# Kernel optimization log

Hardware: AMD Instinct MI355X
Metric: run time of the kernel (lower is better)

The kernel has to match this reference:

```python
import jax, jax.numpy as jnp
import numpy as np
from jax.experimental.ode import odeint

TOL = 1.0  # ODEBlock default: rtol = atol = tol


def _odefunc(x, t, W1, b1, W2, b2):
    # time-concat MLP: f(x, t) = tanh([x, t] @ W1 + b1) @ W2 + b2
    tcol = jnp.full((x.shape[0], 1), t, dtype=x.dtype)  # [B, 1]
    h = jnp.tanh(jnp.concatenate([x, tcol], axis=1) @ W1 + b1)  # [B, H]
    return h @ W2 + b2  # [B, D]


def setup_inputs() -> dict:
    key = jax.random.key(0)
    k1, k2, k3 = jax.random.split(key, 3)
    B, D, H = 4096, 2048, 2048
    # scale weights so the dynamics stay well-conditioned over t in [0,1]
    x = jax.random.normal(k1, (B, D), dtype=jnp.float32)
    W1 = jax.random.normal(k2, (D + 1, H), dtype=jnp.float32) / np.sqrt(D + 1)
    b1 = jnp.zeros((H,), dtype=jnp.float32)
    W2 = jax.random.normal(k3, (H, D), dtype=jnp.float32) / np.sqrt(H)
    b2 = jnp.zeros((D,), dtype=jnp.float32)
    return {"x": x, "W1": W1, "b1": b1, "W2": W2, "b2": b2}


def reference(x, W1, b1, W2, b2):
    f = lambda y, t: _odefunc(y, t, W1, b1, W2, b2)
    ts = jnp.array([0.0, 1.0], dtype=jnp.float32)
    states = odeint(f, x, ts, rtol=TOL, atol=TOL)  # [2, B, D]
    return states[-1]
```

## Files before the change

kernel.cpp:

```cpp
#include <hip/hip_runtime.h>

typedef unsigned short u16;
typedef __attribute__((ext_vector_type(8))) short short8;
typedef __attribute__((ext_vector_type(4))) float floatx4;
typedef __attribute__((ext_vector_type(4))) unsigned short ushortx4;

#define BD 4096
#define DD 2048
#define NTOT (BD*DD)
#define MAX_STEPS 3

#define CE0 ((float)(35.0/384.0 - 1951.0/21600.0))
#define CE2 ((float)(500.0/1113.0 - 22642.0/50085.0))
#define CE3 ((float)(125.0/192.0 - 451.0/720.0))
#define CE4 ((float)(-2187.0/6784.0 + 12231.0/42400.0))
#define CE5 ((float)(11.0/84.0 - 649.0/6300.0))
#define CE6 ((float)(-1.0/60.0))

#define CM0 ((float)(6025192743.0/30085553152.0/2.0))
#define CM2 ((float)(51252292925.0/65400821598.0/2.0))
#define CM3 ((float)(-2691868925.0/45128329728.0/2.0))
#define CM4 ((float)(187940372067.0/1594534317056.0/2.0))
#define CM5 ((float)(-1776094331.0/19743644256.0/2.0))
#define CM6 ((float)(11237099.0/235043384.0/2.0))

#define CS0 ((float)(35.0/384.0))
#define CS2 ((float)(500.0/1113.0))
#define CS3 ((float)(125.0/192.0))
#define CS4 ((float)(-2187.0/6784.0))
#define CS5 ((float)(11.0/84.0))

#define B50 ((float)(9017.0/3168.0))
#define B51 ((float)(-355.0/33.0))
#define B52 ((float)(46732.0/5247.0))
#define B53 ((float)(49.0/176.0))
#define B54 ((float)(-5103.0/18656.0))

struct Scal {
  float t, dt, last_t, h0, dt_saved;
  float d0s, d1s, d2s, errs;
  float d0, d1;
  int run_flag, accept_flag, cur;
};

__device__ __forceinline__ u16 f2bf(float x) {
  unsigned int u = __float_as_uint(x);
  u += 0x7FFFu + ((u >> 16) & 1u);
  return (u16)(u >> 16);
}
__device__ __forceinline__ float bf2f(u16 h) {
  return __uint_as_float(((unsigned int)h) << 16);
}
__device__ __forceinline__ void splitw(float v, u16* oh, u16* ol, size_t idx) {
  u16 h = f2bf(v);
  oh[idx] = h;
  ol[idx] = f2bf(v - bf2f(h));
}
__device__ __forceinline__ void splitw4(floatx4 v, u16* oh, u16* ol, size_t idx) {
  ushortx4 h, l;
  #pragma unroll
  for (int e = 0; e < 4; ++e) {
    u16 hh = f2bf(v[e]);
    h[e] = hh;
    l[e] = f2bf(v[e] - bf2f(hh));
  }
  *(ushortx4*)&oh[idx] = h;
  *(ushortx4*)&ol[idx] = l;
}

__device__ __forceinline__ void gload16(const u16* g, u16* l) {
  __builtin_amdgcn_global_load_lds(
      (const __attribute__((address_space(1))) void*)g,
      (__attribute__((address_space(3))) void*)l, 16, 0, 0);
}

__global__ void transpose_hi(const float* __restrict__ W, u16* __restrict__ th,
                             int K, int N) {
  __shared__ float tile[32][33];
  int k0 = blockIdx.x * 32, n0 = blockIdx.y * 32;
  int tx = threadIdx.x, ty = threadIdx.y;
  #pragma unroll
  for (int j = 0; j < 32; j += 8)
    tile[ty + j][tx] = W[(size_t)(k0 + ty + j) * N + n0 + tx];
  __syncthreads();
  #pragma unroll
  for (int j = 0; j < 32; j += 8) {
    int nn = ty + j, kk = tx;
    th[(size_t)(n0 + nn) * K + k0 + kk] = f2bf(tile[kk][nn]);
  }
}

template <int STAGE>
__global__ __launch_bounds__(256, 2)
void gemm_fused(const u16* __restrict__ Ah, const u16* __restrict__ Al,
                const u16* __restrict__ Bt,
                const float* __restrict__ bias, const float* __restrict__ trow,
                int tmode, float alpha_c,
                float bb0, float bb1, float bb2, float bbv,
                float* __restrict__ YA, float* __restrict__ YB,
                float* __restrict__ F,
                float* __restrict__ K2M, float* __restrict__ K3,
                float* __restrict__ K4,
                u16* __restrict__ oh, u16* __restrict__ ol,
                Scal* __restrict__ s, int flag) {
  if (flag == 1 && !s->run_flag) return;

  __shared__ __attribute__((aligned(16))) u16 raw[2][16384];
  #define AH_OFF 0
  #define AL_OFF 4096
  #define B_OFF  8192

  const int tid = threadIdx.x;
  const int lane = tid & 63;
  const int wave = tid >> 6;

  const int lin = blockIdx.x;
  const int xcd = lin & 7;
  const int slot = lin >> 3;
  const int bm = (xcd * 8 + (slot >> 4)) * 64;
  const int bn = (slot & 15) * 128;

  const int m_w = (wave >> 1) * 32;
  const int n_w = (wave & 1) * 64;
  const int lr = lane & 15;

  const int lrow = lane >> 3;
  const int lcol = (((lane & 7) ^ (lane >> 3)) << 3);
  const int ra = wave * 16;
  const int rb = wave * 32;
  const u16* gAh = Ah + (size_t)(bm + ra + lrow) * DD + lcol;
  const u16* gAl = Al + (size_t)(bm + ra + lrow) * DD + lcol;
  const u16* gB  = Bt + (size_t)(bn + rb + lrow) * DD + lcol;

  floatx4 acc[2][4];
  #pragma unroll
  for (int i = 0; i < 2; ++i)
    #pragma unroll
    for (int j = 0; j < 4; ++j)
      acc[i][j] = (floatx4){0.f, 0.f, 0.f, 0.f};

  auto stage = [&](int k0, int b) {
    #pragma unroll
    for (int t = 0; t < 2; ++t) {
      gload16(gAh + k0 + (size_t)(8 * t) * DD, &raw[b][AH_OFF + (ra + 8 * t) * 64]);
      gload16(gAl + k0 + (size_t)(8 * t) * DD, &raw[b][AL_OFF + (ra + 8 * t) * 64]);
    }
    #pragma unroll
    for (int t = 0; t < 4; ++t)
      gload16(gB + k0 + (size_t)(8 * t) * DD, &raw[b][B_OFF + (rb + 8 * t) * 64]);
  };

  stage(0, 0);
  stage(64, 1);
  asm volatile("s_waitcnt vmcnt(8)" ::: "memory");
  __builtin_amdgcn_s_barrier();

  const int NT = DD / 64;
  int bufc = 0;
  for (int t = 0; t < NT; ++t) {
    #pragma unroll
    for (int kk = 0; kk < 2; ++kk) {
      const int cb = kk * 4 + (lane >> 4);
      short8 afh[2], afl[2], bfv[4];
      #pragma unroll
      for (int i = 0; i < 2; ++i) {
        int r = m_w + i * 16 + lr;
        int ar = r * 64 + ((cb ^ (lr & 7)) << 3);
        afh[i] = *(const short8*)&raw[bufc][AH_OFF + ar];
        afl[i] = *(const short8*)&raw[bufc][AL_OFF + ar];
      }
      #pragma unroll
      for (int j = 0; j < 4; ++j) {
        int r = n_w + j * 16 + lr;
        bfv[j] = *(const short8*)&raw[bufc][B_OFF + r * 64 + ((cb ^ (lr & 7)) << 3)];
      }
      #pragma unroll
      for (int i = 0; i < 2; ++i)
        #pragma unroll
        for (int j = 0; j < 4; ++j) {
          acc[i][j] = __builtin_amdgcn_mfma_f32_16x16x32_bf16(afh[i], bfv[j], acc[i][j], 0, 0, 0);
          acc[i][j] = __builtin_amdgcn_mfma_f32_16x16x32_bf16(afl[i], bfv[j], acc[i][j], 0, 0, 0);
        }
    }

    if (t < NT - 1) {
      __builtin_amdgcn_s_barrier();
      if (t < NT - 2) {
        stage((t + 2) * 64, bufc);
        asm volatile("s_waitcnt vmcnt(8)" ::: "memory");
      } else {
        asm volatile("s_waitcnt vmcnt(0)" ::: "memory");
      }
      __builtin_amdgcn_s_barrier();
      bufc ^= 1;
    }
  }

  const int cur = s->cur;
  const float* Yc = cur ? YB : YA;
  float* NY = cur ? YA : YB;
  const float dt = s->dt;
  float tj = 0.f;
  if (STAGE == 100) tj = (tmode == 0) ? (s->t + dt * alpha_c) : s->h0;

  __syncthreads();
  float* ep = (float*)&raw[0][0];
  const int oq = (lane >> 4) * 4;
  const int oc = lane & 15;
  #pragma unroll
  for (int i = 0; i < 2; ++i)
    #pragma unroll
    for (int j = 0; j < 4; ++j)
      #pragma unroll
      for (int r = 0; r < 4; ++r)
        ep[(m_w + i * 16 + oq + r) * 132 + (n_w + j * 16 + oc)] = acc[i][j][r];
  __syncthreads();

  float err_acc = 0.f;
  #pragma unroll
  for (int q = 0; q < 8; ++q) {
    const int fidx = tid + 256 * q;
    const int rl = fidx >> 5;
    const int cl = (fidx & 31) << 2;
    const int n = bn + cl;
    const size_t idx = (size_t)(bm + rl) * DD + n;
    floatx4 v = *(const floatx4*)&ep[rl * 132 + cl];
    {
      floatx4 b4 = *(const floatx4*)&bias[n];
      #pragma unroll
      for (int e = 0; e < 4; ++e) v[e] = v[e] + b4[e];
    }
    if constexpr (STAGE == 100) {
      floatx4 t4 = *(const floatx4*)&trow[n];
      floatx4 h4;
      #pragma unroll
      for (int e = 0; e < 4; ++e) h4[e] = tanhf(v[e] + tj * t4[e]);
      splitw4(h4, oh, ol, idx);
    } else if constexpr (STAGE == 0) {
      floatx4 fv = *(const floatx4*)&F[idx];
      floatx4 yv = *(const floatx4*)&Yc[idx];
      *(floatx4*)&K2M[idx] = v;
      floatx4 ys;
      #pragma unroll
      for (int e = 0; e < 4; ++e)
        ys[e] = yv[e] + dt * (bb0 * fv[e] + bbv * v[e]);
      splitw4(ys, oh, ol, idx);
    } else if constexpr (STAGE == 1) {
      floatx4 fv = *(const floatx4*)&F[idx];
      floatx4 yv = *(const floatx4*)&Yc[idx];
      floatx4 k2 = *(const floatx4*)&K2M[idx];
      *(floatx4*)&K3[idx] = v;
      floatx4 ys;
      #pragma unroll
      for (int e = 0; e < 4; ++e)
        ys[e] = yv[e] + dt * (bb0 * fv[e] + bb1 * k2[e] + bbv * v[e]);
      splitw4(ys, oh, ol, idx);
    } else if constexpr (STAGE == 2) {
      floatx4 fv = *(const floatx4*)&F[idx];
      floatx4 yv = *(const floatx4*)&Yc[idx];
      floatx4 k2 = *(const floatx4*)&K2M[idx];
      floatx4 k3 = *(const floatx4*)&K3[idx];
      *(floatx4*)&K4[idx] = v;
      floatx4 ys;
      #pragma unroll
      for (int e = 0; e < 4; ++e)
        ys[e] = yv[e] + dt * (bb0 * fv[e] + bb1 * k2[e] + bb2 * k3[e] + bbv * v[e]);
      splitw4(ys, oh, ol, idx);
    } else if constexpr (STAGE == 3) {
      floatx4 fv = *(const floatx4*)&F[idx];
      floatx4 yv = *(const floatx4*)&Yc[idx];
      floatx4 k2 = *(const floatx4*)&K2M[idx];
      floatx4 k3 = *(const floatx4*)&K3[idx];
      floatx4 k4 = *(const floatx4*)&K4[idx];
      *(floatx4*)&K2M[idx] = v;
      floatx4 ys;
      #pragma unroll
      for (int e = 0; e < 4; ++e)
        ys[e] = yv[e] + dt * (B50 * fv[e] + B51 * k2[e] + B52 * k3[e] + B53 * k4[e] + B54 * v[e]);
      splitw4(ys, oh, ol, idx);
    } else if constexpr (STAGE == 4) {
      floatx4 fv = *(const floatx4*)&F[idx];
      floatx4 yv = *(const floatx4*)&Yc[idx];
      floatx4 k3 = *(const floatx4*)&K3[idx];
      floatx4 k4 = *(const floatx4*)&K4[idx];
      floatx4 k5 = *(const floatx4*)&K2M[idx];
      floatx4 ny, E4, M4;
      #pragma unroll
      for (int e = 0; e < 4; ++e) {
        ny[e] = yv[e] + dt * (CS0 * fv[e] + CS2 * k3[e] + CS3 * k4[e] + CS4 * k5[e] + CS5 * v[e]);
        E4[e] = CE0 * fv[e] + CE2 * k3[e] + CE3 * k4[e] + CE4 * k5[e] + CE5 * v[e];
        M4[e] = CM0 * fv[e] + CM2 * k3[e] + CM3 * k4[e] + CM4 * k5[e] + CM5 * v[e];
      }
      *(floatx4*)&NY[idx] = ny;
      *(floatx4*)&K3[idx] = E4;
      *(floatx4*)&K2M[idx] = M4;
      splitw4(ny, oh, ol, idx);
    } else if constexpr (STAGE == 5) {
      floatx4 E4 = *(const floatx4*)&K3[idx];
      floatx4 M4 = *(const floatx4*)&K2M[idx];
      floatx4 yv = *(const floatx4*)&Yc[idx];
      floatx4 nyv = *(const floatx4*)&NY[idx];
      floatx4 Ef, Mf;
      #pragma unroll
      for (int e = 0; e < 4; ++e) {
        Ef[e] = E4[e] + CE6 * v[e];
        Mf[e] = M4[e] + CM6 * v[e];
        float er = dt * Ef[e];
        float tol = 1.f + fmaxf(fabsf(yv[e]), fabsf(nyv[e]));
        float rr = er / tol;
        err_acc += rr * rr;
      }
      *(floatx4*)&K3[idx] = Ef;
      *(floatx4*)&K2M[idx] = Mf;
      *(floatx4*)&K4[idx] = v;
    } else if constexpr (STAGE == 10) {
      *(floatx4*)&F[idx] = v;
    } else {
      *(floatx4*)&K4[idx] = v;
    }
  }

  if constexpr (STAGE == 5) {
    __syncthreads();
    float* red = (float*)&raw[0][0];
    red[tid] = err_acc;
    __syncthreads();
    for (int off = 128; off > 0; off >>= 1) {
      if (tid < off) red[tid] += red[tid + off];
      __syncthreads();
    }
    if (tid == 0) atomicAdd(&s->errs, red[0]);
  }
}

__global__ void k_init_scal(Scal* s) {
  s->t = 0.f; s->dt = 0.f; s->last_t = 0.f; s->h0 = 0.f; s->dt_saved = 1.f;
  s->d0s = 0.f; s->d1s = 0.f; s->d2s = 0.f; s->errs = 0.f;
  s->d0 = 0.f; s->d1 = 0.f;
  s->run_flag = 0; s->accept_flag = 0; s->cur = 0;
}

__global__ void k_init_y(const float* __restrict__ x, float* __restrict__ y,
                         u16* __restrict__ ysh, u16* __restrict__ ysl, int n) {
  for (int i = blockIdx.x * blockDim.x + threadIdx.x; i < n; i += gridDim.x * blockDim.x) {
    float v = x[i];
    y[i] = v;
    splitw(v, ysh, ysl, i);
  }
}

__global__ void k_probe_ys(const float* __restrict__ y, const float* __restrict__ f,
                           u16* __restrict__ ysh, u16* __restrict__ ysl, int n,
                           const Scal* __restrict__ s) {
  float h0 = s->h0;
  for (int i = blockIdx.x * blockDim.x + threadIdx.x; i < n; i += gridDim.x * blockDim.x)
    splitw(y[i] + h0 * f[i], ysh, ysl, i);
}

__global__ void k_prep(float* YA, float* YB, float* __restrict__ F,
                       float* __restrict__ K3p, const float* __restrict__ K4p,
                       float* __restrict__ K2M,
                       u16* __restrict__ ysh, u16* __restrict__ ysl, int n,
                       const Scal* __restrict__ s, int mode) {
  if (mode == 0 && !s->run_flag) return;
  int acc = (mode == 0) ? s->accept_flag : 0;
  int cur = s->cur;
  const float* Yc = cur ? YB : YA;
  const float* Yn = cur ? YA : YB;
  float dtn = s->dt, dts = s->dt_saved;
  for (int i = blockIdx.x * blockDim.x + threadIdx.x; i < n; i += gridDim.x * blockDim.x) {
    float fold = F[i];
    float fnew, ynext;
    if (acc) {
      fnew = K4p[i];
      ynext = Yn[i];
      F[i] = fnew;
      K3p[i] = fold;
      K2M[i] = Yc[i] + dts * K2M[i];
    } else {
      fnew = fold;
      ynext = Yc[i];
    }
    splitw(ynext + dtn * 0.2f * fnew, ysh, ysl, i);
  }
}

__global__ void k_d01(const float* __restrict__ y, const float* __restrict__ f,
                      int n, Scal* s) {
  float a0 = 0.f, a1 = 0.f;
  for (int i = blockIdx.x * blockDim.x + threadIdx.x; i < n; i += gridDim.x * blockDim.x) {
    float yv = y[i], fv = f[i];
    float sc = 1.f + fabsf(yv);
    float t0 = yv / sc, t1 = fv / sc;
    a0 += t0 * t0;
    a1 += t1 * t1;
  }
  __shared__ float r0[256], r1[256];
  int tid = threadIdx.x;
  r0[tid] = a0; r1[tid] = a1;
  __syncthreads();
  for (int off = 128; off > 0; off >>= 1) {
    if (tid < off) { r0[tid] += r0[tid + off]; r1[tid] += r1[tid + off]; }
    __syncthreads();
  }
  if (tid == 0) { atomicAdd(&s->d0s, r0[0]); atomicAdd(&s->d1s, r1[0]); }
}

__global__ void k_h0(Scal* s) {
  float d0 = sqrtf(s->d0s);
  float d1 = sqrtf(s->d1s);
  s->d0 = d0; s->d1 = d1;
  s->h0 = (d0 < 1e-5f || d1 < 1e-5f) ? 1e-6f : 0.01f * d0 / d1;
}

__global__ void k_d2(const float* __restrict__ y, const float* __restrict__ f,
                     const float* __restrict__ f1h, int n, Scal* s) {
  float a = 0.f;
  for (int i = blockIdx.x * blockDim.x + threadIdx.x; i < n; i += gridDim.x * blockDim.x) {
    float v = (f1h[i] - f[i]) / (1.f + fabsf(y[i]));
    a += v * v;
  }
  __shared__ float r0[256];
  int tid = threadIdx.x;
  r0[tid] = a;
  __syncthreads();
  for (int off = 128; off > 0; off >>= 1) {
    if (tid < off) r0[tid] += r0[tid + off];
    __syncthreads();
  }
  if (tid == 0) atomicAdd(&s->d2s, r0[0]);
}

__global__ void k_dt(Scal* s) {
  float d2 = sqrtf(s->d2s) / s->h0;
  float h1 = (s->d1 <= 1e-15f && d2 <= 1e-15f)
                 ? fmaxf(1e-6f, s->h0 * 1e-3f)
                 : powf(0.01f / fmaxf(s->d1, d2), 1.0f / 6.0f);
  s->dt = fminf(100.f * s->h0, h1);
  s->t = 0.f;
  s->last_t = 0.f;
}

__global__ void k_step_begin(Scal* s) {
  s->run_flag = (s->t < 1.0f) && (s->dt > 0.f);
  s->accept_flag = 0;
  s->errs = 0.f;
}

__global__ void k_step_end(Scal* s) {
  if (!s->run_flag) { s->accept_flag = 0; return; }
  float ratio = sqrtf(s->errs / (float)NTOT);
  int acc = (ratio <= 1.0f);
  s->accept_flag = acc;
  float dfactor = (ratio < 1.f) ? 1.f : 0.2f;
  float factor = fminf(10.f, fmaxf(0.9f * powf(ratio, -0.2f), dfactor));
  float ndt = (ratio == 0.f) ? s->dt * 10.f : s->dt * factor;
  if (ndt < 0.f) ndt = 0.f;
  if (acc) { s->dt_saved = s->dt; s->last_t = s->t; s->t = s->t + s->dt; }
  s->dt = ndt;
}

__global__ void k_flip(Scal* s) {
  if (s->accept_flag) s->cur ^= 1;
}

__global__ void k_final(const float* YA, const float* YB,
    const float* __restrict__ f0s, const float* __restrict__ f1s,
    float* out, int n, const Scal* s) {
  int cur = s->cur;
  const float* y1s = cur ? YB : YA;
  const float* y0s = cur ? YA : YB;
  float dt = s->dt_saved;
  float r = (1.0f - s->last_t) / (s->t - s->last_t);
  for (int i = blockIdx.x * blockDim.x + threadIdx.x; i < n; i += gridDim.x * blockDim.x) {
    float y0 = y0s[i], y1 = y1s[i], ym = out[i], f0 = f0s[i], f1 = f1s[i];
    float a = 2.f * dt * (f1 - f0) - 8.f * (y1 + y0) + 16.f * ym;
    float b = dt * (5.f * f0 - 3.f * f1) + 18.f * y0 + 14.f * y1 - 32.f * ym;
    float c = dt * (f1 - 4.f * f0) - 11.f * y0 - 5.f * y1 + 16.f * ym;
    float d = dt * f0;
    out[i] = (((a * r + b) * r + c) * r + d) * r + y0;
  }
}

__global__ void k_debug_ws(float* __restrict__ out, int n, float mb) {
  for (int i = blockIdx.x * blockDim.x + threadIdx.x; i < n; i += gridDim.x * blockDim.x)
    out[i] = mb;
}

extern "C" void kernel_launch(void* const* d_in, const int* in_sizes, int n_in,
                              void* d_out, int out_size, void* d_ws, size_t ws_size,
                              hipStream_t stream) {
  const float* x  = (const float*)d_in[0];
  const float* W1 = (const float*)d_in[1];
  const float* b1 = (const float*)d_in[2];
  const float* W2 = (const float*)d_in[3];
  const float* b2 = (const float*)d_in[4];
  float* out = (float*)d_out;
  const float* w1row = W1 + (size_t)2048 * 2048;

  const size_t SZW = (size_t)2048 * 2048 * 2;
  const size_t SZH = (size_t)NTOT * 2;
  const size_t SZF = (size_t)NTOT * 4;
  const size_t NEED = 1024 + 2 * SZW + 4 * SZH + 5 * SZF;

  if (ws_size < NEED) {
    k_debug_ws<<<2048, 256, 0, stream>>>(out, NTOT, (float)(ws_size >> 20));
    return;
  }

  char* base = (char*)d_ws;
  Scal* s = (Scal*)base;
  size_t o = 1024;
  auto take = [&](size_t bytes) { void* p = base + o; o += bytes; return p; };

  u16* W1T = (u16*)take(SZW); u16* W2T = (u16*)take(SZW);
  u16* YSH = (u16*)take(SZH); u16* YSL = (u16*)take(SZH);
  u16* HH  = (u16*)take(SZH); u16* HL  = (u16*)take(SZH);
  float* YA = (float*)take(SZF); float* YB = (float*)take(SZF);
  float* F  = (float*)take(SZF);
  float* K3 = (float*)take(SZF); float* K4 = (float*)take(SZF);
  float* K2M = out;

  const dim3 GG(1024), GB(256);
  const dim3 EG(2048), EB(256);

  #define G1(tmode, alpha, flag) \
    gemm_fused<100><<<GG, GB, 0, stream>>>(YSH, YSL, W1T, b1, w1row, \
        tmode, alpha, 0.f, 0.f, 0.f, 0.f, \
        YA, YB, F, K2M, K3, K4, HH, HL, s, flag)
  #define G2(st, b0, b1c, b2c, bv, flag) \
    gemm_fused<st><<<GG, GB, 0, stream>>>(HH, HL, W2T, b2, nullptr, \
        0, 0.f, b0, b1c, b2c, bv, \
        YA, YB, F, K2M, K3, K4, YSH, YSL, s, flag)

  transpose_hi<<<dim3(64, 64), dim3(32, 8), 0, stream>>>(W1, W1T, 2048, 2048);
  transpose_hi<<<dim3(64, 64), dim3(32, 8), 0, stream>>>(W2, W2T, 2048, 2048);
  k_init_scal<<<1, 1, 0, stream>>>(s);
  k_init_y<<<EG, EB, 0, stream>>>(x, YA, YSH, YSL, NTOT);

  G1(0, 0.f, 0); G2(10, 0.f, 0.f, 0.f, 0.f, 0);
  k_d01<<<1024, 256, 0, stream>>>(YA, F, NTOT, s);
  k_h0<<<1, 1, 0, stream>>>(s);
  k_probe_ys<<<EG, EB, 0, stream>>>(YA, F, YSH, YSL, NTOT, s);
  G1(1, 0.f, 0); G2(11, 0.f, 0.f, 0.f, 0.f, 0);
  k_d2<<<1024, 256, 0, stream>>>(YA, F, K4, NTOT, s);
  k_dt<<<1, 1, 0, stream>>>(s);
  k_prep<<<EG, EB, 0, stream>>>(YA, YB, F, K3, K4, K2M, YSH, YSL, NTOT, s, 1);

  for (int st = 0; st < MAX_STEPS; ++st) {
    k_step_begin<<<1, 1, 0, stream>>>(s);
    G1(0, 0.2f, 1);
    G2(0, (float)(3.0/40.0), 0.f, 0.f, (float)(9.0/40.0), 1);
    G1(0, 0.3f, 1);
    G2(1, (float)(44.0/45.0), (float)(-56.0/15.0), 0.f, (float)(32.0/9.0), 1);
    G1(0, 0.8f, 1);
    G2(2, (float)(19372.0/6561.0), (float)(-25360.0/2187.0),
       (float)(64448.0/6561.0), (float)(-212.0/729.0), 1);
    G1(0, (float)(8.0/9.0), 1);
    G2(3, 0.f, 0.f, 0.f, 0.f, 1);
    G1(0, 1.f, 1);
    G2(4, 0.f, 0.f, 0.f, 0.f, 1);
    G1(0, 1.f, 1);
    G2(5, 0.f, 0.f, 0.f, 0.f, 1);

    k_step_end<<<1, 1, 0, stream>>>(s);
    k_prep<<<EG, EB, 0, stream>>>(YA, YB, F, K3, K4, K2M, YSH, YSL, NTOT, s, 0);
    k_flip<<<1, 1, 0, stream>>>(s);
  }

  k_final<<<EG, EB, 0, stream>>>(YA, YB, K3, F, out, NTOT, s);

  #undef G1
  #undef G2
}
```

Before: 2.604 ms.

## Halve GEMM K-tile to 32 and raise occupancy to four blocks per CU

The fused GEMM K-step drops from 64 to 32. This shrinks the double-buffered LDS footprint from 64KB to about 33KB, and the launch bounds now target 4 blocks per CU instead of 2. Global-to-LDS staging, the XOR swizzle and the wait counts are reworked for 32-wide rows. The aim is more resident waves to hide memory latency, at the cost of twice as many barriers per K loop and possible register pressure or spills under the tighter occupancy bound.

```diff
diff --git a/kernel.cpp b/kernel.cpp
--- a/kernel.cpp
+++ b/kernel.cpp
@@ -91,7 +91,7 @@
 }
 
 template <int STAGE>
-__global__ __launch_bounds__(256, 2)
+__global__ __launch_bounds__(256, 4)
 void gemm_fused(const u16* __restrict__ Ah, const u16* __restrict__ Al,
                 const u16* __restrict__ Bt,
                 const float* __restrict__ bias, const float* __restrict__ trow,
@@ -105,10 +105,10 @@
                 Scal* __restrict__ s, int flag) {
   if (flag == 1 && !s->run_flag) return;
 
-  __shared__ __attribute__((aligned(16))) u16 raw[2][16384];
-  #define AH_OFF 0
-  #define AL_OFF 4096
-  #define B_OFF  8192
+  __shared__ __attribute__((aligned(16))) u16 raw[16896];
+  #define BUF_STRIDE 8192
+  #define AL_OFF 2048
+  #define B_OFF  4096
 
   const int tid = threadIdx.x;
   const int lane = tid & 63;
@@ -124,8 +124,8 @@
   const int n_w = (wave & 1) * 64;
   const int lr = lane & 15;
 
-  const int lrow = lane >> 3;
-  const int lcol = (((lane & 7) ^ (lane >> 3)) << 3);
+  const int lrow = lane >> 2;
+  const int lcol = (((lane & 3) ^ ((lane >> 3) & 3)) << 3);
   const int ra = wave * 16;
   const int rb = wave * 32;
   const u16* gAh = Ah + (size_t)(bm + ra + lrow) * DD + lcol;
@@ -140,54 +140,49 @@
       acc[i][j] = (floatx4){0.f, 0.f, 0.f, 0.f};
 
   auto stage = [&](int k0, int b) {
-    #pragma unroll
-    for (int t = 0; t < 2; ++t) {
-      gload16(gAh + k0 + (size_t)(8 * t) * DD, &raw[b][AH_OFF + (ra + 8 * t) * 64]);
-      gload16(gAl + k0 + (size_t)(8 * t) * DD, &raw[b][AL_OFF + (ra + 8 * t) * 64]);
-    }
-    #pragma unroll
-    for (int t = 0; t < 4; ++t)
-      gload16(gB + k0 + (size_t)(8 * t) * DD, &raw[b][B_OFF + (rb + 8 * t) * 64]);
+    gload16(gAh + k0, &raw[b * BUF_STRIDE + ra * 32]);
+    gload16(gAl + k0, &raw[b * BUF_STRIDE + AL_OFF + ra * 32]);
+    gload16(gB + k0,  &raw[b * BUF_STRIDE + B_OFF + rb * 32]);
+    gload16(gB + k0 + (size_t)16 * DD,
+            &raw[b * BUF_STRIDE + B_OFF + (rb + 16) * 32]);
   };
 
   stage(0, 0);
-  stage(64, 1);
-  asm volatile("s_waitcnt vmcnt(8)" ::: "memory");
+  stage(32, 1);
+  asm volatile("s_waitcnt vmcnt(4)" ::: "memory");
   __builtin_amdgcn_s_barrier();
 
-  const int NT = DD / 64;
+  const int NT = DD / 32;
   int bufc = 0;
   for (int t = 0; t < NT; ++t) {
+    const int cb = lane >> 4;
+    const int sw = ((lr >> 1) & 3);
+    short8 afh[2], afl[2], bfv[4];
     #pragma unroll
-    for (int kk = 0; kk < 2; ++kk) {
-      const int cb = kk * 4 + (lane >> 4);
-      short8 afh[2], afl[2], bfv[4];
-      #pragma unroll
-      for (int i = 0; i < 2; ++i) {
-        int r = m_w + i * 16 + lr;
-        int ar = r * 64 + ((cb ^ (lr & 7)) << 3);
-        afh[i] = *(const short8*)&raw[bufc][AH_OFF + ar];
-        afl[i] = *(const short8*)&raw[bufc][AL_OFF + ar];
+    for (int i = 0; i < 2; ++i) {
+      int r = m_w + i * 16 + lr;
+      int ar = r * 32 + ((cb ^ sw) << 3);
+      afh[i] = *(const short8*)&raw[bufc * BUF_STRIDE + ar];
+      afl[i] = *(const short8*)&raw[bufc * BUF_STRIDE + AL_OFF + ar];
+    }
+    #pragma unroll
+    for (int j = 0; j < 4; ++j) {
+      int r = n_w + j * 16 + lr;
+      bfv[j] = *(const short8*)&raw[bufc * BUF_STRIDE + B_OFF + r * 32 + ((cb ^ sw) << 3)];
+    }
+    #pragma unroll
+    for (int i = 0; i < 2; ++i)
+      #pragma unroll
+      for (int j = 0; j < 4; ++j) {
+        acc[i][j] = __builtin_amdgcn_mfma_f32_16x16x32_bf16(afh[i], bfv[j], acc[i][j], 0, 0, 0);
+        acc[i][j] = __builtin_amdgcn_mfma_f32_16x16x32_bf16(afl[i], bfv[j], acc[i][j], 0, 0, 0);
       }
-      #pragma unroll
-      for (int j = 0; j < 4; ++j) {
-        int r = n_w + j * 16 + lr;
-        bfv[j] = *(const short8*)&raw[bufc][B_OFF + r * 64 + ((cb ^ (lr & 7)) << 3)];
-      }
-      #pragma unroll
-      for (int i = 0; i < 2; ++i)
-        #pragma unroll
-        for (int j = 0; j < 4; ++j) {
-          acc[i][j] = __builtin_amdgcn_mfma_f32_16x16x32_bf16(afh[i], bfv[j], acc[i][j], 0, 0, 0);
-          acc[i][j] = __builtin_amdgcn_mfma_f32_16x16x32_bf16(afl[i], bfv[j], acc[i][j], 0, 0, 0);
-        }
-    }
 
     if (t < NT - 1) {
       __builtin_amdgcn_s_barrier();
       if (t < NT - 2) {
-        stage((t + 2) * 64, bufc);
-        asm volatile("s_waitcnt vmcnt(8)" ::: "memory");
+        stage((t + 2) * 32, bufc);
+        asm volatile("s_waitcnt vmcnt(4)" ::: "memory");
       } else {
         asm volatile("s_waitcnt vmcnt(0)" ::: "memory");
       }
@@ -204,7 +199,7 @@
   if (STAGE == 100) tj = (tmode == 0) ? (s->t + dt * alpha_c) : s->h0;
 
   __syncthreads();
-  float* ep = (float*)&raw[0][0];
+  float* ep = (float*)&raw[0];
   const int oq = (lane >> 4) * 4;
   const int oc = lane & 15;
   #pragma unroll
@@ -322,7 +317,7 @@
 
   if constexpr (STAGE == 5) {
     __syncthreads();
-    float* red = (float*)&raw[0][0];
+    float* red = (float*)&raw[0];
     red[tid] = err_acc;
     __syncthreads();
     for (int off = 128; off > 0; off >>= 1) {
@@ -331,6 +326,9 @@
     }
     if (tid == 0) atomicAdd(&s->errs, red[0]);
   }
+  #undef BUF_STRIDE
+  #undef AL_OFF
+  #undef B_OFF
 }
 
 __global__ void k_init_scal(Scal* s) {
```

New measurement: 2.854 ms. 9.6% more time.

## Store RK stage derivatives as bf16 and defer error/midpoint combos to final stage

Applied to the files above, without the earlier changes.

The Dormand-Prince stage derivatives (F, k2..k6) are now stored as bf16 instead of fp32, which halves the bytes moved in every GEMM epilogue and in the prep, probe and norm kernels. The error and midpoint combinations are no longer accumulated across stages 4 and 5; stage 4 stores k6 and stage 5 computes both combinations from all stored stages at once. k_prep is vectorised to process four elements per thread. The exchange is lower precision in the derivative terms used for the stage updates, the error estimate and the final interpolation.

```diff
diff --git a/kernel.cpp b/kernel.cpp
--- a/kernel.cpp
+++ b/kernel.cpp
@@ -66,6 +66,19 @@
   }
   *(ushortx4*)&oh[idx] = h;
   *(ushortx4*)&ol[idx] = l;
+}
+__device__ __forceinline__ floatx4 load4bf(const u16* __restrict__ p, size_t idx) {
+  ushortx4 u = *(const ushortx4*)&p[idx];
+  floatx4 f;
+  #pragma unroll
+  for (int e = 0; e < 4; ++e) f[e] = bf2f(u[e]);
+  return f;
+}
+__device__ __forceinline__ void store4bf(u16* __restrict__ p, size_t idx, floatx4 v) {
+  ushortx4 u;
+  #pragma unroll
+  for (int e = 0; e < 4; ++e) u[e] = f2bf(v[e]);
+  *(ushortx4*)&p[idx] = u;
 }
 
 __device__ __forceinline__ void gload16(const u16* g, u16* l) {
@@ -98,9 +111,9 @@
                 int tmode, float alpha_c,
                 float bb0, float bb1, float bb2, float bbv,
                 float* __restrict__ YA, float* __restrict__ YB,
-                float* __restrict__ F,
-                float* __restrict__ K2M, float* __restrict__ K3,
-                float* __restrict__ K4,
+                u16* __restrict__ FB, u16* __restrict__ KB2,
+                u16* __restrict__ KB3, u16* __restrict__ KB4,
+                u16* __restrict__ KB6, float* __restrict__ Mout,
                 u16* __restrict__ oh, u16* __restrict__ ol,
                 Scal* __restrict__ s, int flag) {
   if (flag == 1 && !s->run_flag) return;
@@ -237,86 +250,84 @@
       for (int e = 0; e < 4; ++e) h4[e] = tanhf(v[e] + tj * t4[e]);
       splitw4(h4, oh, ol, idx);
     } else if constexpr (STAGE == 0) {
-      floatx4 fv = *(const floatx4*)&F[idx];
+      floatx4 fv = load4bf(FB, idx);
       floatx4 yv = *(const floatx4*)&Yc[idx];
-      *(floatx4*)&K2M[idx] = v;
+      store4bf(KB2, idx, v);
       floatx4 ys;
       #pragma unroll
       for (int e = 0; e < 4; ++e)
         ys[e] = yv[e] + dt * (bb0 * fv[e] + bbv * v[e]);
       splitw4(ys, oh, ol, idx);
     } else if constexpr (STAGE == 1) {
-      floatx4 fv = *(const floatx4*)&F[idx];
+      floatx4 fv = load4bf(FB, idx);
       floatx4 yv = *(const floatx4*)&Yc[idx];
-      floatx4 k2 = *(const floatx4*)&K2M[idx];
-      *(floatx4*)&K3[idx] = v;
+      floatx4 k2 = load4bf(KB2, idx);
+      store4bf(KB3, idx, v);
       floatx4 ys;
       #pragma unroll
       for (int e = 0; e < 4; ++e)
         ys[e] = yv[e] + dt * (bb0 * fv[e] + bb1 * k2[e] + bbv * v[e]);
       splitw4(ys, oh, ol, idx);
     } else if constexpr (STAGE == 2) {
-      floatx4 fv = *(const floatx4*)&F[idx];
+      floatx4 fv = load4bf(FB, idx);
       floatx4 yv = *(const floatx4*)&Yc[idx];
-      floatx4 k2 = *(const floatx4*)&K2M[idx];
-      floatx4 k3 = *(const floatx4*)&K3[idx];
-      *(floatx4*)&K4[idx] = v;
+      floatx4 k2 = load4bf(KB2, idx);
+      floatx4 k3 = load4bf(KB3, idx);
+      store4bf(KB4, idx, v);
       floatx4 ys;
       #pragma unroll
       for (int e = 0; e < 4; ++e)
         ys[e] = yv[e] + dt * (bb0 * fv[e] + bb1 * k2[e] + bb2 * k3[e] + bbv * v[e]);
       splitw4(ys, oh, ol, idx);
     } else if constexpr (STAGE == 3) {
-      floatx4 fv = *(const floatx4*)&F[idx];
+      floatx4 fv = load4bf(FB, idx);
       floatx4 yv = *(const floatx4*)&Yc[idx];
-      floatx4 k2 = *(const floatx4*)&K2M[idx];
-      floatx4 k3 = *(const floatx4*)&K3[idx];
-      floatx4 k4 = *(const floatx4*)&K4[idx];
-      *(floatx4*)&K2M[idx] = v;
+      floatx4 k2 = load4bf(KB2, idx);
+      floatx4 k3 = load4bf(KB3, idx);
+      floatx4 k4 = load4bf(KB4, idx);
+      store4bf(KB2, idx, v);
       floatx4 ys;
       #pragma unroll
       for (int e = 0; e < 4; ++e)
         ys[e] = yv[e] + dt * (B50 * fv[e] + B51 * k2[e] + B52 * k3[e] + B53 * k4[e] + B54 * v[e]);
       splitw4(ys, oh, ol, idx);
     } else if constexpr (STAGE == 4) {
-      floatx4 fv = *(const floatx4*)&F[idx];
+      floatx4 fv = load4bf(FB, idx);
       floatx4 yv = *(const floatx4*)&Yc[idx];
-      floatx4 k3 = *(const floatx4*)&K3[idx];
-      floatx4 k4 = *(const floatx4*)&K4[idx];
-      floatx4 k5 = *(const floatx4*)&K2M[idx];
-      floatx4 ny, E4, M4;
-      #pragma unroll
-      for (int e = 0; e < 4; ++e) {
+      floatx4 k3 = load4bf(KB3, idx);
+      floatx4 k4 = load4bf(KB4, idx);
+      floatx4 k5 = load4bf(KB2, idx);
+      floatx4 ny;
+      #pragma unroll
+      for (int e = 0; e < 4; ++e)
         ny[e] = yv[e] + dt * (CS0 * fv[e] + CS2 * k3[e] + CS3 * k4[e] + CS4 * k5[e] + CS5 * v[e]);
-        E4[e] = CE0 * fv[e] + CE2 * k3[e] + CE3 * k4[e] + CE4 * k5[e] + CE5 * v[e];
-        M4[e] = CM0 * fv[e] + CM2 * k3[e] + CM3 * k4[e] + CM4 * k5[e] + CM5 * v[e];
-      }
       *(floatx4*)&NY[idx] = ny;
-      *(floatx4*)&K3[idx] = E4;
-      *(floatx4*)&K2M[idx] = M4;
+      store4bf(KB6, idx, v);
       splitw4(ny, oh, ol, idx);
     } else if constexpr (STAGE == 5) {
-      floatx4 E4 = *(const floatx4*)&K3[idx];
-      floatx4 M4 = *(const floatx4*)&K2M[idx];
+      floatx4 fv = load4bf(FB, idx);
+      floatx4 k3 = load4bf(KB3, idx);
+      floatx4 k4 = load4bf(KB4, idx);
+      floatx4 k5 = load4bf(KB2, idx);
+      floatx4 k6 = load4bf(KB6, idx);
       floatx4 yv = *(const floatx4*)&Yc[idx];
       floatx4 nyv = *(const floatx4*)&NY[idx];
-      floatx4 Ef, Mf;
+      floatx4 M4;
       #pragma unroll
       for (int e = 0; e < 4; ++e) {
-        Ef[e] = E4[e] + CE6 * v[e];
-        Mf[e] = M4[e] + CM6 * v[e];
-        float er = dt * Ef[e];
+        float Ef = CE0 * fv[e] + CE2 * k3[e] + CE3 * k4[e] + CE4 * k5[e] + CE5 * k6[e] + CE6 * v[e];
+        M4[e] = CM0 * fv[e] + CM2 * k3[e] + CM3 * k4[e] + CM4 * k5[e] + CM5 * k6[e] + CM6 * v[e];
+        float er = dt * Ef;
         float tol = 1.f + fmaxf(fabsf(yv[e]), fabsf(nyv[e]));
         float rr = er / tol;
         err_acc += rr * rr;
       }
-      *(floatx4*)&K3[idx] = Ef;
-      *(floatx4*)&K2M[idx] = Mf;
-      *(floatx4*)&K4[idx] = v;
+      store4bf(KB4, idx, v);
+      *(floatx4*)&Mout[idx] = M4;
     } else if constexpr (STAGE == 10) {
-      *(floatx4*)&F[idx] = v;
+      store4bf(FB, idx, v);
     } else {
-      *(floatx4*)&K4[idx] = v;
+      store4bf(KB4, idx, v);
     }
   }
 
@@ -331,6 +342,9 @@
     }
     if (tid == 0) atomicAdd(&s->errs, red[0]);
   }
+  #undef AH_OFF
+  #undef AL_OFF
+  #undef B_OFF
 }
 
 __global__ void k_init_scal(Scal* s) {
@@ -349,18 +363,18 @@
   }
 }
 
-__global__ void k_probe_ys(const float* __restrict__ y, const float* __restrict__ f,
+__global__ void k_probe_ys(const float* __restrict__ y, const u16* __restrict__ fb,
                            u16* __restrict__ ysh, u16* __restrict__ ysl, int n,
                            const Scal* __restrict__ s) {
   float h0 = s->h0;
   for (int i = blockIdx.x * blockDim.x + threadIdx.x; i < n; i += gridDim.x * blockDim.x)
-    splitw(y[i] + h0 * f[i], ysh, ysl, i);
-}
-
-__global__ void k_prep(float* YA, float* YB, float* __restrict__ F,
-                       float* __restrict__ K3p, const float* __restrict__ K4p,
-                       float* __restrict__ K2M,
-                       u16* __restrict__ ysh, u16* __restrict__ ysl, int n,
+    splitw(y[i] + h0 * bf2f(fb[i]), ysh, ysl, i);
+}
+
+__global__ void k_prep(float* YA, float* YB, u16* __restrict__ FB,
+                       u16* __restrict__ KB3, const u16* __restrict__ KB4,
+                       float* __restrict__ Mout,
+                       u16* __restrict__ ysh, u16* __restrict__ ysl, int n4,
                        const Scal* __restrict__ s, int mode) {
   if (mode == 0 && !s->run_flag) return;
   int acc = (mode == 0) ? s->accept_flag : 0;
@@ -368,28 +382,37 @@
   const float* Yc = cur ? YB : YA;
   const float* Yn = cur ? YA : YB;
   float dtn = s->dt, dts = s->dt_saved;
-  for (int i = blockIdx.x * blockDim.x + threadIdx.x; i < n; i += gridDim.x * blockDim.x) {
-    float fold = F[i];
-    float fnew, ynext;
+  for (int i = blockIdx.x * blockDim.x + threadIdx.x; i < n4; i += gridDim.x * blockDim.x) {
+    size_t idx = (size_t)i * 4;
+    ushortx4 fold = *(const ushortx4*)&FB[idx];
+    floatx4 ys;
     if (acc) {
-      fnew = K4p[i];
-      ynext = Yn[i];
-      F[i] = fnew;
-      K3p[i] = fold;
-      K2M[i] = Yc[i] + dts * K2M[i];
+      ushortx4 k7 = *(const ushortx4*)&KB4[idx];
+      floatx4 yn4 = *(const floatx4*)&Yn[idx];
+      floatx4 yc4 = *(const floatx4*)&Yc[idx];
+      floatx4 m4 = *(const floatx4*)&Mout[idx];
+      *(ushortx4*)&FB[idx] = k7;
+      *(ushortx4*)&KB3[idx] = fold;
+      floatx4 ym;
+      #pragma unroll
+      for (int e = 0; e < 4; ++e) ym[e] = yc4[e] + dts * m4[e];
+      *(floatx4*)&Mout[idx] = ym;
+      #pragma unroll
+      for (int e = 0; e < 4; ++e) ys[e] = yn4[e] + dtn * 0.2f * bf2f(k7[e]);
     } else {
-      fnew = fold;
-      ynext = Yc[i];
+      floatx4 yc4 = *(const floatx4*)&Yc[idx];
+      #pragma unroll
+      for (int e = 0; e < 4; ++e) ys[e] = yc4[e] + dtn * 0.2f * bf2f(fold[e]);
     }
-    splitw(ynext + dtn * 0.2f * fnew, ysh, ysl, i);
-  }
-}
-
-__global__ void k_d01(const float* __restrict__ y, const float* __restrict__ f,
+    splitw4(ys, ysh, ysl, idx);
+  }
+}
+
+__global__ void k_d01(const float* __restrict__ y, const u16* __restrict__ fb,
                       int n, Scal* s) {
   float a0 = 0.f, a1 = 0.f;
   for (int i = blockIdx.x * blockDim.x + threadIdx.x; i < n; i += gridDim.x * blockDim.x) {
-    float yv = y[i], fv = f[i];
+    float yv = y[i], fv = bf2f(fb[i]);
     float sc = 1.f + fabsf(yv);
     float t0 = yv / sc, t1 = fv / sc;
     a0 += t0 * t0;
@@ -413,11 +436,11 @@
   s->h0 = (d0 < 1e-5f || d1 < 1e-5f) ? 1e-6f : 0.01f * d0 / d1;
 }
 
-__global__ void k_d2(const float* __restrict__ y, const float* __restrict__ f,
-                     const float* __restrict__ f1h, int n, Scal* s) {
+__global__ void k_d2(const float* __restrict__ y, const u16* __restrict__ fb,
+                     const u16* __restrict__ f1h, int n, Scal* s) {
   float a = 0.f;
   for (int i = blockIdx.x * blockDim.x + threadIdx.x; i < n; i += gridDim.x * blockDim.x) {
-    float v = (f1h[i] - f[i]) / (1.f + fabsf(y[i]));
+    float v = (bf2f(f1h[i]) - bf2f(fb[i])) / (1.f + fabsf(y[i]));
     a += v * v;
   }
   __shared__ float r0[256];
@@ -465,7 +488,7 @@
 }
 
 __global__ void k_final(const float* YA, const float* YB,
-    const float* __restrict__ f0s, const float* __restrict__ f1s,
+    const u16* __restrict__ f0s, const u16* __restrict__ f1s,
     float* out, int n, const Scal* s) {
   int cur = s->cur;
   const float* y1s = cur ? YB : YA;
@@ -473,7 +496,8 @@
   float dt = s->dt_saved;
   float r = (1.0f - s->last_t) / (s->t - s->last_t);
   for (int i = blockIdx.x * blockDim.x + threadIdx.x; i < n; i += gridDim.x * blockDim.x) {
-    float y0 = y0s[i], y1 = y1s[i], ym = out[i], f0 = f0s[i], f1 = f1s[i];
+    float y0 = y0s[i], y1 = y1s[i], ym = out[i];
+    float f0 = bf2f(f0s[i]), f1 = bf2f(f1s[i]);
     float a = 2.f * dt * (f1 - f0) - 8.f * (y1 + y0) + 16.f * ym;
     float b = dt * (5.f * f0 - 3.f * f1) + 18.f * y0 + 14.f * y1 - 32.f * ym;
     float c = dt * (f1 - 4.f * f0) - 11.f * y0 - 5.f * y1 + 16.f * ym;
@@ -501,7 +525,7 @@
   const size_t SZW = (size_t)2048 * 2048 * 2;
   const size_t SZH = (size_t)NTOT * 2;
   const size_t SZF = (size_t)NTOT * 4;
-  const size_t NEED = 1024 + 2 * SZW + 4 * SZH + 5 * SZF;
+  const size_t NEED = 1024 + 2 * SZW + 4 * SZH + 2 * SZF + 5 * SZH;
 
   if (ws_size < NEED) {
     k_debug_ws<<<2048, 256, 0, stream>>>(out, NTOT, (float)(ws_size >> 20));
@@ -517,9 +541,10 @@
   u16* YSH = (u16*)take(SZH); u16* YSL = (u16*)take(SZH);
   u16* HH  = (u16*)take(SZH); u16* HL  = (u16*)take(SZH);
   float* YA = (float*)take(SZF); float* YB = (float*)take(SZF);
-  float* F  = (float*)take(SZF);
-  float* K3 = (float*)take(SZF); float* K4 = (float*)take(SZF);
-  float* K2M = out;
+  u16* FB  = (u16*)take(SZH); u16* KB2 = (u16*)take(SZH);
+  u16* KB3 = (u16*)take(SZH); u16* KB4 = (u16*)take(SZH);
+  u16* KB6 = (u16*)take(SZH);
+  float* Mout = out;
 
   const dim3 GG(1024), GB(256);
   const dim3 EG(2048), EB(256);
@@ -527,11 +552,11 @@
   #define G1(tmode, alpha, flag) \
     gemm_fused<100><<<GG, GB, 0, stream>>>(YSH, YSL, W1T, b1, w1row, \
         tmode, alpha, 0.f, 0.f, 0.f, 0.f, \
-        YA, YB, F, K2M, K3, K4, HH, HL, s, flag)
+        YA, YB, FB, KB2, KB3, KB4, KB6, Mout, HH, HL, s, flag)
   #define G2(st, b0, b1c, b2c, bv, flag) \
     gemm_fused<st><<<GG, GB, 0, stream>>>(HH, HL, W2T, b2, nullptr, \
         0, 0.f, b0, b1c, b2c, bv, \
-        YA, YB, F, K2M, K3, K4, YSH, YSL, s, flag)
+        YA, YB, FB, KB2, KB3, KB4, KB6, Mout, YSH, YSL, s, flag)
 
   transpose_hi<<<dim3(64, 64), dim3(32, 8), 0, stream>>>(W1, W1T, 2048, 2048);
   transpose_hi<<<dim3(64, 64), dim3(32, 8), 0, stream>>>(W2, W2T, 2048, 2048);
@@ -539,13 +564,13 @@
   k_init_y<<<EG, EB, 0, stream>>>(x, YA, YSH, YSL, NTOT);
 
   G1(0, 0.f, 0); G2(10, 0.f, 0.f, 0.f, 0.f, 0);
-  k_d01<<<1024, 256, 0, stream>>>(YA, F, NTOT, s);
+  k_d01<<<1024, 256, 0, stream>>>(YA, FB, NTOT, s);
   k_h0<<<1, 1, 0, stream>>>(s);
-  k_probe_ys<<<EG, EB, 0, stream>>>(YA, F, YSH, YSL, NTOT, s);
+  k_probe_ys<<<EG, EB, 0, stream>>>(YA, FB, YSH, YSL, NTOT, s);
   G1(1, 0.f, 0); G2(11, 0.f, 0.f, 0.f, 0.f, 0);
-  k_d2<<<1024, 256, 0, stream>>>(YA, F, K4, NTOT, s);
+  k_d2<<<1024, 256, 0, stream>>>(YA, FB, KB4, NTOT, s);
   k_dt<<<1, 1, 0, stream>>>(s);
-  k_prep<<<EG, EB, 0, stream>>>(YA, YB, F, K3, K4, K2M, YSH, YSL, NTOT, s, 1);
+  k_prep<<<EG, EB, 0, stream>>>(YA, YB, FB, KB3, KB4, Mout, YSH, YSL, NTOT / 4, s, 1);
 
   for (int st = 0; st < MAX_STEPS; ++st) {
     k_step_begin<<<1, 1, 0, stream>>>(s);
@@ -564,11 +589,11 @@
     G2(5, 0.f, 0.f, 0.f, 0.f, 1);
 
     k_step_end<<<1, 1, 0, stream>>>(s);
-    k_prep<<<EG, EB, 0, stream>>>(YA, YB, F, K3, K4, K2M, YSH, YSL, NTOT, s, 0);
+    k_prep<<<EG, EB, 0, stream>>>(YA, YB, FB, KB3, KB4, Mout, YSH, YSL, NTOT / 4, s, 0);
     k_flip<<<1, 1, 0, stream>>>(s);
   }
 
-  k_final<<<EG, EB, 0, stream>>>(YA, YB, K3, F, out, NTOT, s);
+  k_final<<<EG, EB, 0, stream>>>(YA, YB, KB3, FB, out, NTOT, s);
 
   #undef G1
   #undef G2
```

After: 2.383 ms, median of 2. 8.5% less time.
